# Kernel optimization log

Hardware: AMD Instinct MI355X
Metric: run time of the kernel (lower is better)

Reference implementation:

```python
import jax, jax.numpy as jnp
import numpy as np

B, T, D, O, E = 4, 4096, 256, 256, 16


def setup_inputs() -> dict:
    key = jax.random.key(0)
    ks = jax.random.split(key, 5)
    s_in = 1.0 / np.sqrt(D)
    x = jax.random.normal(ks[0], (B, T, D), dtype=jnp.float32)
    We = jax.random.uniform(ks[1], (E, D, O), minval=-s_in, maxval=s_in, dtype=jnp.float32)
    be = jax.random.uniform(ks[2], (E, O), minval=-s_in, maxval=s_in, dtype=jnp.float32)
    Wg = jax.random.uniform(ks[3], (D, E), minval=-s_in, maxval=s_in, dtype=jnp.float32)
    bg = jax.random.uniform(ks[4], (E,), minval=-s_in, maxval=s_in, dtype=jnp.float32)
    return {"x": x, "We": We, "be": be, "Wg": Wg, "bg": bg}


def reference(x, We, be, Wg, bg):
    # gate: softmax over experts  [B,T,E]
    gate = jax.nn.softmax(jnp.einsum("btd,de->bte", x, Wg) + bg, axis=-1)
    # all experts: batched GEMM  [B,T,E,O]
    h = jax.nn.gelu(jnp.einsum("btd,edo->bteo", x, We) + be, approximate=False)
    # softmax-weighted sum over experts  [B,T,O]
    return jnp.einsum("bteo,bte->bto", h, gate)
```

## Files before the change

### kernel.cpp

```cpp
#include <hip/hip_runtime.h>
#include <stdint.h>

#define KD 256
#define NO 256
#define NE 16
#define BM 64
#define BN 128
#define BKK 64
#define WROW 72
#define XROW 264
#define NIT 64

typedef short bf16x8 __attribute__((ext_vector_type(8)));
typedef float f32x4 __attribute__((ext_vector_type(4)));

__device__ __forceinline__ unsigned short f2bf(float f) {
  uint32_t u = __float_as_uint(f);
  u += 0x7fffu + ((u >> 16) & 1u);
  return (unsigned short)(u >> 16);
}
__device__ __forceinline__ float bf2f(unsigned short h) {
  return __uint_as_float(((uint32_t)h) << 16);
}
__device__ __forceinline__ float gelu_f(float h) {
  float z = h * fmaf(0.07135481627f, h * h, 1.5957691216f);
  return h * __builtin_amdgcn_rcpf(1.0f + __expf(-z));
}

__global__ void moe_prep(const float* __restrict__ We, unsigned short* __restrict__ Wt,
                         const float* __restrict__ Wg, unsigned short* __restrict__ Wgt)
{
  __shared__ float ts[64 * 65];
  const int tid = threadIdx.x;
  const int bid = blockIdx.x;
  if (bid < 256) {
    int e = bid >> 4;
    int d0 = ((bid >> 2) & 3) * 64;
    int o0 = (bid & 3) * 64;
    int c = tid & 63, rg = tid >> 6;
    const float* src = We + ((size_t)e * KD + d0) * NO + o0;
#pragma unroll
    for (int i = 0; i < 16; ++i) {
      int r = i * 4 + rg;
      ts[c * 65 + r] = src[r * NO + c];
    }
    __syncthreads();
    unsigned short* dst = Wt + ((size_t)e * NO + o0) * KD + d0;
#pragma unroll
    for (int i = 0; i < 16; ++i) {
      int o = i * 4 + rg;
      dst[o * KD + c] = f2bf(ts[o * 65 + c]);
    }
  } else {
    int d = tid;
    const float* wr = Wg + (size_t)d * NE;
#pragma unroll
    for (int e = 0; e < NE; ++e)
      Wgt[e * KD + d] = f2bf(wr[e]);
  }
}

__launch_bounds__(256, 2)
__global__ void moe_main(const float* __restrict__ x,
                         const unsigned short* __restrict__ Wt,
                         const unsigned short* __restrict__ Wgt,
                         const float* __restrict__ be,
                         const float* __restrict__ bg,
                         float* __restrict__ out)
{
  __shared__ __align__(16) unsigned short u_lds[2 * BN * WROW];
  __shared__ float gate_t[NE * 65];
  __shared__ unsigned short be_h[NE * BN];

  const int tid = threadIdx.x;
  const int bid = blockIdx.x;
  const int n0 = (bid & 1) * BN;
  const int m0 = (bid >> 1) * BM;
  const int wid = tid >> 6, lane = tid & 63;
  const int wm = wid >> 1, wn = wid & 1;
  const int ln = lane & 15, quad = lane >> 4;

  const int srow = tid >> 3;
  const int spj = tid & 7;
  auto wgsrc = [&](int t, int pass) -> const uint4* {
    int e = t >> 2, kc = t & 3;
    int row = pass * 32 + srow;
    return (const uint4*)(Wt + (((size_t)e * NO + n0 + row) * KD + kc * BKK + spj * 8));
  };

  uint4 w0 = *wgsrc(0, 0), w1 = *wgsrc(0, 1), w2 = *wgsrc(0, 2), w3 = *wgsrc(0, 3);

  {
    const float4* xg = (const float4*)x + (size_t)m0 * (KD / 4);
#pragma unroll
    for (int p = 0; p < 16; ++p) {
      int idx = p * 256 + tid;
      int r = idx >> 6, c = idx & 63;
      float4 v = xg[r * (KD / 4) + c];
      uint32_t lo = (uint32_t)f2bf(v.x) | ((uint32_t)f2bf(v.y) << 16);
      uint32_t hi = (uint32_t)f2bf(v.z) | ((uint32_t)f2bf(v.w) << 16);
      *(uint2*)&u_lds[r * XROW + c * 4] = make_uint2(lo, hi);
    }
  }
#pragma unroll
  for (int p = 0; p < 8; ++p) {
    int idx = p * 256 + tid;
    int e = idx >> 7, c = idx & 127;
    be_h[e * BN + c] = f2bf(be[e * NO + n0 + c]);
  }
  __syncthreads();

  bf16x8 a[2][8];
  const int arow = wm * 32 + ln;
#pragma unroll
  for (int i = 0; i < 2; ++i)
#pragma unroll
    for (int kc = 0; kc < 8; ++kc)
      a[i][kc] = *(const bf16x8*)&u_lds[(arow + i * 16) * XROW + kc * 32 + quad * 8];

  {
    f32x4 g0 = {0.f, 0.f, 0.f, 0.f}, g1 = {0.f, 0.f, 0.f, 0.f};
#pragma unroll
    for (int kc = 0; kc < 8; ++kc) {
      bf16x8 wb = *(const bf16x8*)(Wgt + (size_t)ln * KD + kc * 32 + quad * 8);
      g0 = __builtin_amdgcn_mfma_f32_16x16x32_bf16(a[0][kc], wb, g0, 0, 0, 0);
      g1 = __builtin_amdgcn_mfma_f32_16x16x32_bf16(a[1][kc], wb, g1, 0, 0, 0);
    }
    float bgl = bg[ln];
#pragma unroll
    for (int i = 0; i < 2; ++i)
#pragma unroll
      for (int r = 0; r < 4; ++r) {
        float v = (i == 0 ? g0[r] : g1[r]) + bgl;
        float mx = v;
#pragma unroll
        for (int msk = 1; msk < 16; msk <<= 1)
          mx = fmaxf(mx, __shfl_xor(mx, msk, 64));
        float ev = __expf(v - mx);
        float s = ev;
#pragma unroll
        for (int msk = 1; msk < 16; msk <<= 1)
          s += __shfl_xor(s, msk, 64);
        float gv = ev * __builtin_amdgcn_rcpf(s);
        if (wn == 0)
          gate_t[ln * 65 + wm * 32 + i * 16 + quad * 4 + r] = gv;
      }
  }
  __syncthreads();

  {
    unsigned short* d = u_lds;
    *(uint4*)&d[(srow +  0) * WROW + spj * 8] = w0;
    *(uint4*)&d[(srow + 32) * WROW + spj * 8] = w1;
    *(uint4*)&d[(srow + 64) * WROW + spj * 8] = w2;
    *(uint4*)&d[(srow + 96) * WROW + spj * 8] = w3;
  }
  w0 = *wgsrc(1, 0); w1 = *wgsrc(1, 1); w2 = *wgsrc(1, 2); w3 = *wgsrc(1, 3);
  __syncthreads();

  f32x4 acc[2][4], oacc[2][4];
#pragma unroll
  for (int i = 0; i < 2; ++i)
#pragma unroll
    for (int j = 0; j < 4; ++j) {
      acc[i][j] = (f32x4){0.f, 0.f, 0.f, 0.f};
      oacc[i][j] = (f32x4){0.f, 0.f, 0.f, 0.f};
    }

  const int brow = wn * 64 + ln;

#pragma unroll 1
  for (int e = 0; e < NE; ++e) {
#pragma unroll
    for (int c = 0; c < 4; ++c) {
      const int t = (e << 2) + c;
      const unsigned short* wb = u_lds + (t & 1) * (BN * WROW);
      if (c < 3 || e < NE - 1) {
        unsigned short* d = u_lds + ((t + 1) & 1) * (BN * WROW);
        *(uint4*)&d[(srow +  0) * WROW + spj * 8] = w0;
        *(uint4*)&d[(srow + 32) * WROW + spj * 8] = w1;
        *(uint4*)&d[(srow + 64) * WROW + spj * 8] = w2;
        *(uint4*)&d[(srow + 96) * WROW + spj * 8] = w3;
      }
      if (t < NIT - 2) {
        w0 = *wgsrc(t + 2, 0); w1 = *wgsrc(t + 2, 1);
        w2 = *wgsrc(t + 2, 2); w3 = *wgsrc(t + 2, 3);
      }
#pragma unroll
      for (int ks = 0; ks < 2; ++ks) {
        bf16x8 b[4];
#pragma unroll
        for (int j = 0; j < 4; ++j)
          b[j] = *(const bf16x8*)&wb[(brow + j * 16) * WROW + ks * 32 + quad * 8];
        const int kc = c * 2 + ks;
#pragma unroll
        for (int i = 0; i < 2; ++i)
#pragma unroll
          for (int j = 0; j < 4; ++j)
            acc[i][j] = __builtin_amdgcn_mfma_f32_16x16x32_bf16(a[i][kc], b[j], acc[i][j], 0, 0, 0);
      }
      __syncthreads();
    }
    {
      float gv[2][4];
#pragma unroll
      for (int i = 0; i < 2; ++i)
#pragma unroll
        for (int r = 0; r < 4; ++r)
          gv[i][r] = gate_t[e * 65 + wm * 32 + i * 16 + quad * 4 + r];
#pragma unroll
      for (int j = 0; j < 4; ++j) {
        float bias = bf2f(be_h[e * BN + brow + j * 16]);
#pragma unroll
        for (int i = 0; i < 2; ++i)
#pragma unroll
          for (int r = 0; r < 4; ++r) {
            float h = acc[i][j][r] + bias;
            oacc[i][j][r] = fmaf(gv[i][r], gelu_f(h), oacc[i][j][r]);
            acc[i][j][r] = 0.f;
          }
      }
    }
  }

#pragma unroll
  for (int i = 0; i < 2; ++i)
#pragma unroll
    for (int r = 0; r < 4; ++r) {
      int row = m0 + wm * 32 + i * 16 + quad * 4 + r;
      float* orow = out + (size_t)row * NO + n0 + wn * 64 + ln;
      orow[0]  = oacc[i][0][r];
      orow[16] = oacc[i][1][r];
      orow[32] = oacc[i][2][r];
      orow[48] = oacc[i][3][r];
    }
}

extern "C" void kernel_launch(void* const* d_in, const int* in_sizes, int n_in,
                              void* d_out, int out_size, void* d_ws, size_t ws_size,
                              hipStream_t stream) {
  const float* x  = (const float*)d_in[0];
  const float* We = (const float*)d_in[1];
  const float* be = (const float*)d_in[2];
  const float* Wg = (const float*)d_in[3];
  const float* bg = (const float*)d_in[4];
  float* out = (float*)d_out;
  unsigned short* Wt  = (unsigned short*)d_ws;
  unsigned short* Wgt = (unsigned short*)((char*)d_ws + (size_t)NE * NO * KD * 2);

  moe_prep<<<257, 256, 0, stream>>>(We, Wt, Wg, Wgt);
  moe_main<<<512, 256, 0, stream>>>(x, Wt, Wgt, be, bg, out);
}
```

Measured before the change: 131.9 us.

## Pre-swizzle expert weights into MFMA fragment order and stream directly to registers

The prep kernel now writes bf16 expert weights in the exact per-lane MFMA B-fragment layout, so each lane can load its fragment with coalesced 16-byte global loads. The main kernel drops the double-buffered LDS staging of weights and the per-chunk __syncthreads, and instead keeps a 4-deep register ring of prefetched fragments. This removes LDS write/read traffic and barriers from the inner loop. In exchange it uses more VGPRs and relies on L2 or global latency being hidden by the register prefetch depth, with the two waves sharing an n-tile each loading their own copy.

```diff
diff --git a/kernel.cpp b/kernel.cpp
--- a/kernel.cpp
+++ b/kernel.cpp
@@ -6,10 +6,8 @@
 #define NE 16
 #define BM 64
 #define BN 128
-#define BKK 64
-#define WROW 72
 #define XROW 264
-#define NIT 64
+#define NFRAG 128
 
 typedef short bf16x8 __attribute__((ext_vector_type(8)));
 typedef float f32x4 __attribute__((ext_vector_type(4)));
@@ -27,29 +25,36 @@
   return h * __builtin_amdgcn_rcpf(1.0f + __expf(-z));
 }
 
-__global__ void moe_prep(const float* __restrict__ We, unsigned short* __restrict__ Wt,
+__global__ void moe_prep(const float* __restrict__ We, unsigned short* __restrict__ Wf,
                          const float* __restrict__ Wg, unsigned short* __restrict__ Wgt)
 {
-  __shared__ float ts[64 * 65];
+  __shared__ float ts[256 * 17];
   const int tid = threadIdx.x;
   const int bid = blockIdx.x;
   if (bid < 256) {
-    int e = bid >> 4;
-    int d0 = ((bid >> 2) & 3) * 64;
-    int o0 = (bid & 3) * 64;
-    int c = tid & 63, rg = tid >> 6;
-    const float* src = We + ((size_t)e * KD + d0) * NO + o0;
-#pragma unroll
-    for (int i = 0; i < 16; ++i) {
-      int r = i * 4 + rg;
-      ts[c * 65 + r] = src[r * NO + c];
+    const int e = bid >> 4, ob = bid & 15;
+    const float* src = We + (size_t)e * KD * NO + ob * 16;
+    const int o = tid & 15, dg = tid >> 4;
+#pragma unroll
+    for (int p = 0; p < 16; ++p) {
+      int d = p * 16 + dg;
+      ts[d * 17 + o] = src[(size_t)d * NO + o];
     }
     __syncthreads();
-    unsigned short* dst = Wt + ((size_t)e * NO + o0) * KD + d0;
-#pragma unroll
-    for (int i = 0; i < 16; ++i) {
-      int o = i * 4 + rg;
-      dst[o * KD + c] = f2bf(ts[o * 65 + c]);
+    const int w = tid >> 6, l = tid & 63;
+    const int q = l >> 4, ln = l & 15;
+#pragma unroll
+    for (int kk = 0; kk < 2; ++kk) {
+      int kc = w + kk * 4;
+      unsigned int pk[4];
+#pragma unroll
+      for (int h = 0; h < 4; ++h) {
+        unsigned short lo = f2bf(ts[(kc * 32 + q * 8 + h * 2 + 0) * 17 + ln]);
+        unsigned short hi = f2bf(ts[(kc * 32 + q * 8 + h * 2 + 1) * 17 + ln]);
+        pk[h] = (unsigned int)lo | ((unsigned int)hi << 16);
+      }
+      uint4* dst = (uint4*)(Wf + ((((size_t)(e * 8 + kc) * 16 + ob) * 64) + l) * 8);
+      *dst = make_uint4(pk[0], pk[1], pk[2], pk[3]);
     }
   } else {
     int d = tid;
@@ -62,33 +67,26 @@
 
 __launch_bounds__(256, 2)
 __global__ void moe_main(const float* __restrict__ x,
-                         const unsigned short* __restrict__ Wt,
+                         const uint4* __restrict__ Wf,
                          const unsigned short* __restrict__ Wgt,
                          const float* __restrict__ be,
                          const float* __restrict__ bg,
                          float* __restrict__ out)
 {
-  __shared__ __align__(16) unsigned short u_lds[2 * BN * WROW];
+  __shared__ __align__(16) unsigned short Xs[BM * XROW];
   __shared__ float gate_t[NE * 65];
   __shared__ unsigned short be_h[NE * BN];
 
   const int tid = threadIdx.x;
   const int bid = blockIdx.x;
-  const int n0 = (bid & 1) * BN;
+  const int half = bid & 1;
+  const int n0 = half * BN;
   const int m0 = (bid >> 1) * BM;
   const int wid = tid >> 6, lane = tid & 63;
   const int wm = wid >> 1, wn = wid & 1;
   const int ln = lane & 15, quad = lane >> 4;
 
-  const int srow = tid >> 3;
-  const int spj = tid & 7;
-  auto wgsrc = [&](int t, int pass) -> const uint4* {
-    int e = t >> 2, kc = t & 3;
-    int row = pass * 32 + srow;
-    return (const uint4*)(Wt + (((size_t)e * NO + n0 + row) * KD + kc * BKK + spj * 8));
-  };
-
-  uint4 w0 = *wgsrc(0, 0), w1 = *wgsrc(0, 1), w2 = *wgsrc(0, 2), w3 = *wgsrc(0, 3);
+  const int voff = (half * 8 + wn * 4) * 64 + lane;
 
   {
     const float4* xg = (const float4*)x + (size_t)m0 * (KD / 4);
@@ -99,7 +97,7 @@
       float4 v = xg[r * (KD / 4) + c];
       uint32_t lo = (uint32_t)f2bf(v.x) | ((uint32_t)f2bf(v.y) << 16);
       uint32_t hi = (uint32_t)f2bf(v.z) | ((uint32_t)f2bf(v.w) << 16);
-      *(uint2*)&u_lds[r * XROW + c * 4] = make_uint2(lo, hi);
+      *(uint2*)&Xs[r * XROW + c * 4] = make_uint2(lo, hi);
     }
   }
 #pragma unroll
@@ -116,7 +114,14 @@
   for (int i = 0; i < 2; ++i)
 #pragma unroll
     for (int kc = 0; kc < 8; ++kc)
-      a[i][kc] = *(const bf16x8*)&u_lds[(arow + i * 16) * XROW + kc * 32 + quad * 8];
+      a[i][kc] = *(const bf16x8*)&Xs[(arow + i * 16) * XROW + kc * 32 + quad * 8];
+
+  uint4 b[4][4];
+#pragma unroll
+  for (int t = 0; t < 4; ++t) {
+    const uint4* p = Wf + (size_t)t * 1024 + voff;
+    b[t][0] = p[0]; b[t][1] = p[64]; b[t][2] = p[128]; b[t][3] = p[192];
+  }
 
   {
     f32x4 g0 = {0.f, 0.f, 0.f, 0.f}, g1 = {0.f, 0.f, 0.f, 0.f};
@@ -148,16 +153,6 @@
   }
   __syncthreads();
 
-  {
-    unsigned short* d = u_lds;
-    *(uint4*)&d[(srow +  0) * WROW + spj * 8] = w0;
-    *(uint4*)&d[(srow + 32) * WROW + spj * 8] = w1;
-    *(uint4*)&d[(srow + 64) * WROW + spj * 8] = w2;
-    *(uint4*)&d[(srow + 96) * WROW + spj * 8] = w3;
-  }
-  w0 = *wgsrc(1, 0); w1 = *wgsrc(1, 1); w2 = *wgsrc(1, 2); w3 = *wgsrc(1, 3);
-  __syncthreads();
-
   f32x4 acc[2][4], oacc[2][4];
 #pragma unroll
   for (int i = 0; i < 2; ++i)
@@ -167,41 +162,29 @@
       oacc[i][j] = (f32x4){0.f, 0.f, 0.f, 0.f};
     }
 
-  const int brow = wn * 64 + ln;
-
 #pragma unroll 1
   for (int e = 0; e < NE; ++e) {
 #pragma unroll
-    for (int c = 0; c < 4; ++c) {
-      const int t = (e << 2) + c;
-      const unsigned short* wb = u_lds + (t & 1) * (BN * WROW);
-      if (c < 3 || e < NE - 1) {
-        unsigned short* d = u_lds + ((t + 1) & 1) * (BN * WROW);
-        *(uint4*)&d[(srow +  0) * WROW + spj * 8] = w0;
-        *(uint4*)&d[(srow + 32) * WROW + spj * 8] = w1;
-        *(uint4*)&d[(srow + 64) * WROW + spj * 8] = w2;
-        *(uint4*)&d[(srow + 96) * WROW + spj * 8] = w3;
-      }
-      if (t < NIT - 2) {
-        w0 = *wgsrc(t + 2, 0); w1 = *wgsrc(t + 2, 1);
-        w2 = *wgsrc(t + 2, 2); w3 = *wgsrc(t + 2, 3);
-      }
-#pragma unroll
-      for (int ks = 0; ks < 2; ++ks) {
-        bf16x8 b[4];
-#pragma unroll
-        for (int j = 0; j < 4; ++j)
-          b[j] = *(const bf16x8*)&wb[(brow + j * 16) * WROW + ks * 32 + quad * 8];
-        const int kc = c * 2 + ks;
+    for (int h = 0; h < 4; ++h) {
+      const int t = e * 8 + h * 2;
+#pragma unroll
+      for (int s = 0; s < 2; ++s) {
+        const int kc = h * 2 + s;
+        uint4* bc = b[(t + s) & 3];
 #pragma unroll
         for (int i = 0; i < 2; ++i)
 #pragma unroll
           for (int j = 0; j < 4; ++j)
-            acc[i][j] = __builtin_amdgcn_mfma_f32_16x16x32_bf16(a[i][kc], b[j], acc[i][j], 0, 0, 0);
-      }
-      __syncthreads();
+            acc[i][j] = __builtin_amdgcn_mfma_f32_16x16x32_bf16(
+                a[i][kc], *(const bf16x8*)&bc[j], acc[i][j], 0, 0, 0);
+        if (t + s + 4 < NFRAG) {
+          const uint4* p = Wf + (size_t)(t + s + 4) * 1024 + voff;
+          bc[0] = p[0]; bc[1] = p[64]; bc[2] = p[128]; bc[3] = p[192];
+        }
+      }
     }
     {
+      const int brow = wn * 64 + ln;
       float gv[2][4];
 #pragma unroll
       for (int i = 0; i < 2; ++i)
@@ -215,8 +198,8 @@
         for (int i = 0; i < 2; ++i)
 #pragma unroll
           for (int r = 0; r < 4; ++r) {
-            float h = acc[i][j][r] + bias;
-            oacc[i][j][r] = fmaf(gv[i][r], gelu_f(h), oacc[i][j][r]);
+            float hh = acc[i][j][r] + bias;
+            oacc[i][j][r] = fmaf(gv[i][r], gelu_f(hh), oacc[i][j][r]);
             acc[i][j][r] = 0.f;
           }
       }
@@ -245,9 +228,9 @@
   const float* Wg = (const float*)d_in[3];
   const float* bg = (const float*)d_in[4];
   float* out = (float*)d_out;
-  unsigned short* Wt  = (unsigned short*)d_ws;
+  unsigned short* Wf  = (unsigned short*)d_ws;
   unsigned short* Wgt = (unsigned short*)((char*)d_ws + (size_t)NE * NO * KD * 2);
 
-  moe_prep<<<257, 256, 0, stream>>>(We, Wt, Wg, Wgt);
-  moe_main<<<512, 256, 0, stream>>>(x, Wt, Wgt, be, bg, out);
-}
+  moe_prep<<<257, 256, 0, stream>>>(We, Wf, Wg, Wgt);
+  moe_main<<<512, 256, 0, stream>>>(x, (const uint4*)Wf, Wgt, be, bg, out);
+}
```

Result: faster. 127.7 us (-3.2%).
